# Optimization experiments

Hardware: AMD Instinct MI355X
Metric: run time of the kernel (lower is better)

The kernel has to match this reference:

```python
import jax, jax.numpy as jnp
import numpy as np

# Module hyperparameters (from init_kwargs)
NBITS = 8
FOLD = 8
B = 8192
IN_F = 2048
OUT_F = 2048
ISIZE = IN_F // FOLD   # 256
OSIZE = OUT_F // FOLD  # 256
QMAX = 2 ** (NBITS - 1) - 1  # 127


def setup_inputs() -> dict:
    key = jax.random.key(0)
    k1, k2, k3, k4, k5 = jax.random.split(key, 5)
    inp = jax.random.normal(k1, (B, IN_F), dtype=jnp.float32)
    # per-fold linear weights, torch nn.Linear default-ish scale
    W = jax.random.normal(k2, (FOLD, OSIZE, ISIZE), dtype=jnp.float32) * (1.0 / np.sqrt(ISIZE))
    # UniformPositionalEncoding buffers: offset + per-fold per-column ranges
    pe = jax.random.normal(k3, (1, FOLD, ISIZE), dtype=jnp.float32) * 0.1
    min_range = -jax.random.uniform(k4, (1, FOLD, ISIZE), minval=0.25, maxval=1.0, dtype=jnp.float32)
    max_range = jax.random.uniform(k5, (1, FOLD, ISIZE), minval=0.25, maxval=1.0, dtype=jnp.float32)
    return {"input": inp, "W": W, "pe": pe, "min_range": min_range, "max_range": max_range}


def reference(input, W, pe, min_range, max_range):
    b = input.shape[0]
    x = input.reshape(b, FOLD, ISIZE)
    # QuantAct symmetric, clamp_only=True: per-tensor scale s = max|x| / n, clamp to [-s*n, s*n]
    s = jnp.max(jnp.abs(x)) / QMAX
    x = jnp.clip(x, -s * QMAX, s * QMAX)
    s = s * QMAX  # scaled range multiplier
    # positional offset, broadcast over batch
    x = x + pe[0]  # [b, FOLD, ISIZE]
    x_flat = x.reshape(b * FOLD, ISIZE)

    def per_fold(Wi, mn, mx):
        # fold_idx_ste forward passes full x through; range mask zeroes out-of-range entries
        mask = (x_flat < mn * s) | (x_flat > mx * s)  # [b*FOLD, ISIZE]
        xm = jnp.where(mask, jnp.float32(0.0), x_flat)
        o = xm @ Wi.T  # [b*FOLD, OSIZE]
        return o.reshape(b, FOLD, OSIZE).sum(axis=1)  # [b, OSIZE]

    # vmap over the FOLD small linears
    out = jax.vmap(per_fold)(W, min_range[0], max_range[0])  # [FOLD, b, OSIZE]
    out = jnp.transpose(out, (1, 0, 2)).reshape(b, FOLD * OSIZE)  # stack dim=1 then flatten
    return out
```

## Files before the change

### kernel.cpp

```cpp
#include <hip/hip_runtime.h>

#define FOLD  8
#define ISIZE 256
#define IN_F  2048
#define OUT_F 2048
#define TBM   32
#define NBLK  (8192 / TBM)
#define CHW   1104

typedef __attribute__((ext_vector_type(8))) short short8;
typedef __attribute__((ext_vector_type(4))) float f32x4;
typedef __attribute__((ext_vector_type(2))) float f32x2;

__device__ __forceinline__ unsigned f2bf(float f) {
    unsigned u = __float_as_uint(f);
    u += 0x7FFFu + ((u >> 16) & 1u);
    return (u >> 16);
}

__global__ __launch_bounds__(256)
void absmax_conv(const float* __restrict__ in,
                 const float* __restrict__ W,
                 float* __restrict__ partials,
                 unsigned short* __restrict__ wsw,
                 int quota) {
    const int nthreads = gridDim.x * 256;
    const int idx = blockIdx.x * 256 + threadIdx.x;

    if (blockIdx.x < 256) {
        const int t    = blockIdx.x * 256 + threadIdx.x;
        const int wid  = t >> 6;
        const int l    = t & 63;
        const int i  = wid >> 7;
        const int nt = (wid >> 3) & 15;
        const int ks = wid & 7;
        const int n = l & 15, q = l >> 4;
        const float* src = W + (((size_t)i * 256 + nt * 16 + n) * 256 + ks * 32 + q * 8);
        float4 s0 = *(const float4*)(src);
        float4 s1 = *(const float4*)(src + 4);
        uint4 p;
        p.x = f2bf(s0.x) | (f2bf(s0.y) << 16);
        p.y = f2bf(s0.z) | (f2bf(s0.w) << 16);
        p.z = f2bf(s1.x) | (f2bf(s1.y) << 16);
        p.w = f2bf(s1.z) | (f2bf(s1.w) << 16);
        *(uint4*)(wsw + (size_t)wid * 512 + l * 8) = p;
    }

    float m = 0.f;
    #pragma unroll 4
    for (int q = 0; q < quota; ++q) {
        f32x4 a = __builtin_nontemporal_load(
            (const f32x4*)(in + (size_t)(idx + q * nthreads) * 4));
        m = fmaxf(m, fmaxf(fmaxf(fabsf(a[0]), fabsf(a[1])),
                           fmaxf(fabsf(a[2]), fabsf(a[3]))));
    }
    #pragma unroll
    for (int off = 32; off > 0; off >>= 1)
        m = fmaxf(m, __shfl_down(m, off, 64));
    __shared__ float sm[4];
    int lane = threadIdx.x & 63, wv = threadIdx.x >> 6;
    if (lane == 0) sm[wv] = m;
    __syncthreads();
    if (threadIdx.x == 0)
        partials[blockIdx.x] = fmaxf(fmaxf(sm[0], sm[1]), fmaxf(sm[2], sm[3]));
}

__global__ __launch_bounds__(256)
void absmax_kernel(const float4* __restrict__ in,
                   float* __restrict__ partials,
                   unsigned int* __restrict__ scal,
                   int quota, int mode) {
    const int nthreads = gridDim.x * 256;
    const int idx = blockIdx.x * 256 + threadIdx.x;
    float m = 0.f;
    #pragma unroll 4
    for (int q = 0; q < quota; ++q) {
        float4 a = in[idx + q * nthreads];
        m = fmaxf(m, fmaxf(fmaxf(fabsf(a.x), fabsf(a.y)),
                           fmaxf(fabsf(a.z), fabsf(a.w))));
    }
    #pragma unroll
    for (int off = 32; off > 0; off >>= 1)
        m = fmaxf(m, __shfl_down(m, off, 64));
    __shared__ float sm[4];
    int lane = threadIdx.x & 63, wv = threadIdx.x >> 6;
    if (lane == 0) sm[wv] = m;
    __syncthreads();
    if (threadIdx.x == 0) {
        float r = fmaxf(fmaxf(sm[0], sm[1]), fmaxf(sm[2], sm[3]));
        if (mode) partials[blockIdx.x] = r;
        else      atomicMax(scal, __float_as_uint(r));
    }
}

__global__ __launch_bounds__(1024, 1)
void fold_nt(const float* __restrict__ in,
             const unsigned short* __restrict__ wsw,
             const float* __restrict__ pe,
             const float* __restrict__ mn,
             const float* __restrict__ mx,
             const float* __restrict__ partials,
             int npart,
             float* __restrict__ out) {
    __shared__ __align__(16) unsigned short ylds[64 * CHW];
    __shared__ float sred[16];

    const int tid  = threadIdx.x;
    const int lane = tid & 63;
    const int wv   = tid >> 6;
    const int row0 = blockIdx.x * TBM;

    float mabs;
    {
        float v = (tid < npart) ? partials[tid] : 0.0f;
        #pragma unroll
        for (int off = 32; off > 0; off >>= 1)
            v = fmaxf(v, __shfl_down(v, off, 64));
        if (lane == 0) sred[wv] = v;
        __syncthreads();
        float r = sred[0];
        #pragma unroll
        for (int i = 1; i < 16; ++i) r = fmaxf(r, sred[i]);
        mabs = r;
    }
    const float c = (mabs / 127.0f) * 127.0f;

    {
        const int kp  = tid & 127;
        const int rq  = tid >> 7;
        const int k0  = kp * 2;
        const int jh  = kp & 3;
        const int qA  = (kp >> 2) & 3;
        const int ksA = kp >> 4;

        float pef[FOLD][2], lo[FOLD][2], hi[FOLD][2];
        #pragma unroll
        for (int f = 0; f < FOLD; ++f) {
            float2 p2 = *(const float2*)(pe + f * ISIZE + k0);
            pef[f][0] = p2.x; pef[f][1] = p2.y;
        }
        #pragma unroll
        for (int i = 0; i < FOLD; ++i) {
            float2 a2 = *(const float2*)(mn + i * ISIZE + k0);
            float2 b2 = *(const float2*)(mx + i * ISIZE + k0);
            lo[i][0] = a2.x * c; lo[i][1] = a2.y * c;
            hi[i][0] = b2.x * c; hi[i][1] = b2.y * c;
        }

        #pragma unroll
        for (int r4 = 0; r4 < 4; ++r4) {
            const int row = rq * 4 + r4;
            const float* rowp = in + (size_t)(row0 + row) * IN_F + k0;
            f32x2 xr[FOLD];
            #pragma unroll
            for (int f = 0; f < FOLD; ++f)
                xr[f] = __builtin_nontemporal_load((const f32x2*)(rowp + f * ISIZE));

            float acc[FOLD][2];
            #pragma unroll
            for (int i = 0; i < FOLD; ++i) { acc[i][0] = 0.0f; acc[i][1] = 0.0f; }
            #pragma unroll
            for (int f = 0; f < FOLD; ++f) {
                float xv0 = fminf(fmaxf(xr[f][0], -c), c) + pef[f][0];
                float xv1 = fminf(fmaxf(xr[f][1], -c), c) + pef[f][1];
                #pragma unroll
                for (int i = 0; i < FOLD; ++i) {
                    if (xv0 >= lo[i][0] && xv0 <= hi[i][0]) acc[i][0] += xv0;
                    if (xv1 >= lo[i][1] && xv1 <= hi[i][1]) acc[i][1] += xv1;
                }
            }
            const unsigned base = (unsigned)((row >> 4) * 544 + qA * 136 + (row & 15) * 8 + jh * 2);
            #pragma unroll
            for (int i = 0; i < FOLD; ++i) {
                unsigned us = f2bf(acc[i][0]) | (f2bf(acc[i][1]) << 16);
                *(unsigned*)&ylds[(i * 8 + ksA) * CHW + base] = us;
            }
        }
    }
    __syncthreads();

    {
        const int fi   = wv >> 1;
        const int nh   = wv & 1;
        const int mrow = lane & 15;
        const int quad = lane >> 4;

        short8 afr[8][2];
        #pragma unroll
        for (int kk = 0; kk < 8; ++kk) {
            #pragma unroll
            for (int mt = 0; mt < 2; ++mt)
                afr[kk][mt] = *(const short8*)&ylds[(fi * 8 + kk) * CHW + mt * 544 + quad * 136 + mrow * 8];
        }

        const int col0 = fi * 256 + mrow;
        #pragma unroll 2
        for (int nt8 = 0; nt8 < 8; ++nt8) {
            const int ntg = nh * 8 + nt8;
            f32x4 a0 = (f32x4){0.f, 0.f, 0.f, 0.f};
            f32x4 a1 = (f32x4){0.f, 0.f, 0.f, 0.f};
            const unsigned short* wb = wsw + ((size_t)(fi * 16 + ntg) * 8) * 512 + lane * 8;
            uint4 wq[8];
            #pragma unroll
            for (int kk = 0; kk < 8; ++kk) wq[kk] = *(const uint4*)(wb + kk * 512);
            #pragma unroll
            for (int kk = 0; kk < 8; ++kk) {
                union { uint4 u; short8 s; } cv; cv.u = wq[kk];
                a0 = __builtin_amdgcn_mfma_f32_16x16x32_bf16(afr[kk][0], cv.s, a0, 0, 0, 0);
                a1 = __builtin_amdgcn_mfma_f32_16x16x32_bf16(afr[kk][1], cv.s, a1, 0, 0, 0);
            }
            #pragma unroll
            for (int rg = 0; rg < 4; ++rg) {
                __builtin_nontemporal_store(a0[rg],
                    &out[(size_t)(row0 +      quad * 4 + rg) * OUT_F + col0 + ntg * 16]);
                __builtin_nontemporal_store(a1[rg],
                    &out[(size_t)(row0 + 16 + quad * 4 + rg) * OUT_F + col0 + ntg * 16]);
            }
        }
    }
}

__global__ __launch_bounds__(1024, 1)
void fold_main(const float* __restrict__ in,
               const float* __restrict__ W,
               const float* __restrict__ pe,
               const float* __restrict__ mn,
               const float* __restrict__ mx,
               const float* __restrict__ partials,
               const unsigned int* __restrict__ scal,
               int npart,
               float* __restrict__ out) {
    __shared__ __align__(16) unsigned short ylds[64 * CHW];
    __shared__ float sred[16];

    const int tid  = threadIdx.x;
    const int lane = tid & 63;
    const int wv   = tid >> 6;
    const int row0 = blockIdx.x * TBM;

    float mabs;
    if (npart > 0) {
        float v = (tid < npart) ? partials[tid] : 0.0f;
        #pragma unroll
        for (int off = 32; off > 0; off >>= 1)
            v = fmaxf(v, __shfl_down(v, off, 64));
        if (lane == 0) sred[wv] = v;
        __syncthreads();
        float r = sred[0];
        #pragma unroll
        for (int i = 1; i < 16; ++i) r = fmaxf(r, sred[i]);
        mabs = r;
    } else {
        mabs = __uint_as_float(*scal);
    }
    const float c = (mabs / 127.0f) * 127.0f;

    {
        const int kp  = tid & 127;
        const int rq  = tid >> 7;
        const int k0  = kp * 2;
        const int jh  = kp & 3;
        const int qA  = (kp >> 2) & 3;
        const int ksA = kp >> 4;

        float pef[FOLD][2], lo[FOLD][2], hi[FOLD][2];
        #pragma unroll
        for (int f = 0; f < FOLD; ++f) {
            float2 p2 = *(const float2*)(pe + f * ISIZE + k0);
            pef[f][0] = p2.x; pef[f][1] = p2.y;
        }
        #pragma unroll
        for (int i = 0; i < FOLD; ++i) {
            float2 a2 = *(const float2*)(mn + i * ISIZE + k0);
            float2 b2 = *(const float2*)(mx + i * ISIZE + k0);
            lo[i][0] = a2.x * c; lo[i][1] = a2.y * c;
            hi[i][0] = b2.x * c; hi[i][1] = b2.y * c;
        }

        #pragma unroll
        for (int r4 = 0; r4 < 4; ++r4) {
            const int row = rq * 4 + r4;
            const float* rowp = in + (size_t)(row0 + row) * IN_F + k0;
            float2 xr[FOLD];
            #pragma unroll
            for (int f = 0; f < FOLD; ++f) xr[f] = *(const float2*)(rowp + f * ISIZE);

            float acc[FOLD][2];
            #pragma unroll
            for (int i = 0; i < FOLD; ++i) { acc[i][0] = 0.0f; acc[i][1] = 0.0f; }
            #pragma unroll
            for (int f = 0; f < FOLD; ++f) {
                float xv0 = fminf(fmaxf(xr[f].x, -c), c) + pef[f][0];
                float xv1 = fminf(fmaxf(xr[f].y, -c), c) + pef[f][1];
                #pragma unroll
                for (int i = 0; i < FOLD; ++i) {
                    if (xv0 >= lo[i][0] && xv0 <= hi[i][0]) acc[i][0] += xv0;
                    if (xv1 >= lo[i][1] && xv1 <= hi[i][1]) acc[i][1] += xv1;
                }
            }
            const unsigned base = (unsigned)((row >> 4) * 544 + qA * 136 + (row & 15) * 8 + jh * 2);
            #pragma unroll
            for (int i = 0; i < FOLD; ++i) {
                unsigned us = f2bf(acc[i][0]) | (f2bf(acc[i][1]) << 16);
                *(unsigned*)&ylds[(i * 8 + ksA) * CHW + base] = us;
            }
        }
    }
    __syncthreads();

    {
        const int fi   = wv >> 1;
        const int nh   = wv & 1;
        const int mrow = lane & 15;
        const int quad = lane >> 4;

        short8 afr[8][2];
        #pragma unroll
        for (int kk = 0; kk < 8; ++kk) {
            #pragma unroll
            for (int mt = 0; mt < 2; ++mt)
                afr[kk][mt] = *(const short8*)&ylds[(fi * 8 + kk) * CHW + mt * 544 + quad * 136 + mrow * 8];
        }

        const int col0 = fi * 256 + mrow;
        #pragma unroll 2
        for (int nt8 = 0; nt8 < 8; ++nt8) {
            const int ntg = nh * 8 + nt8;
            f32x4 a0 = (f32x4){0.f, 0.f, 0.f, 0.f};
            f32x4 a1 = (f32x4){0.f, 0.f, 0.f, 0.f};
            const float* wb = W + ((size_t)(fi * 256 + ntg * 16 + mrow) * 256 + quad * 8);
            float4 w[16];
            #pragma unroll
            for (int kk = 0; kk < 8; ++kk) {
                w[2 * kk]     = *(const float4*)(wb + kk * 32);
                w[2 * kk + 1] = *(const float4*)(wb + kk * 32 + 4);
            }
            #pragma unroll
            for (int kk = 0; kk < 8; ++kk) {
                union { uint4 u; short8 s; } cv;
                cv.u.x = f2bf(w[2*kk].x)   | (f2bf(w[2*kk].y)   << 16);
                cv.u.y = f2bf(w[2*kk].z)   | (f2bf(w[2*kk].w)   << 16);
                cv.u.z = f2bf(w[2*kk+1].x) | (f2bf(w[2*kk+1].y) << 16);
                cv.u.w = f2bf(w[2*kk+1].z) | (f2bf(w[2*kk+1].w) << 16);
                a0 = __builtin_amdgcn_mfma_f32_16x16x32_bf16(afr[kk][0], cv.s, a0, 0, 0, 0);
                a1 = __builtin_amdgcn_mfma_f32_16x16x32_bf16(afr[kk][1], cv.s, a1, 0, 0, 0);
            }
            #pragma unroll
            for (int rg = 0; rg < 4; ++rg) {
                out[(size_t)(row0 +      quad * 4 + rg) * OUT_F + col0 + ntg * 16] = a0[rg];
                out[(size_t)(row0 + 16 + quad * 4 + rg) * OUT_F + col0 + ntg * 16] = a1[rg];
            }
        }
    }
}

extern "C" void kernel_launch(void* const* d_in, const int* in_sizes, int n_in,
                              void* d_out, int out_size, void* d_ws, size_t ws_size,
                              hipStream_t stream) {
    const float* in = (const float*)d_in[0];
    const float* W  = (const float*)d_in[1];
    const float* pe = (const float*)d_in[2];
    const float* mn = (const float*)d_in[3];
    const float* mx = (const float*)d_in[4];
    float* out = (float*)d_out;

    const size_t PART_OFF  = 16;
    const size_t WSW_OFF   = 8192;
    const size_t WSW_BYTES = (size_t)FOLD * 256 * 256 * 2;

    unsigned int*   scal     = (unsigned int*)d_ws;
    float*          partials = (float*)((char*)d_ws + PART_OFF);
    unsigned short* wsw      = (unsigned short*)((char*)d_ws + WSW_OFF);

    const bool preconv = ws_size >= WSW_OFF + WSW_BYTES;

    if (preconv && ws_size >= PART_OFF + 1024 * sizeof(float)) {
        absmax_conv<<<1024, 256, 0, stream>>>(in, W, partials, wsw, 16);
        fold_nt<<<NBLK, 1024, 0, stream>>>(in, wsw, pe, mn, mx, partials, 1024, out);
        return;
    }

    int npart;
    if (ws_size >= PART_OFF + 1024 * sizeof(float)) {
        absmax_kernel<<<1024, 256, 0, stream>>>((const float4*)in, partials, scal, 16, 1);
        npart = 1024;
    } else if (ws_size >= PART_OFF + 256 * sizeof(float)) {
        absmax_kernel<<<256, 256, 0, stream>>>((const float4*)in, partials, scal, 64, 1);
        npart = 256;
    } else {
        (void)hipMemsetAsync(d_ws, 0, sizeof(unsigned int), stream);
        absmax_kernel<<<256, 256, 0, stream>>>((const float4*)in, partials, scal, 64, 0);
        npart = 0;
    }
    fold_main<<<NBLK, 1024, 0, stream>>>(in, W, pe, mn, mx,
                                         partials, scal, npart, out);
}
```

Measured before the change: 155.1 us.

## Split fold kernel into two 16-row halves with prefetch overlapping MFMA phase

The fused fold kernel now processes its 32-row tile as two 16-row halves in separate LDS buffers. Input rows for the second half are prefetched into registers before the first half's MFMA/store phase, then masked and converted after it. The aim is to overlap global input loads with matrix work and output stores instead of running them back to back. In exchange each weight tile is loaded twice per block, there is an extra barrier, and range parameters are reloaded, which raises register pressure.

```diff
diff --git a/kernel.cpp b/kernel.cpp
--- a/kernel.cpp
+++ b/kernel.cpp
@@ -7,6 +7,8 @@
 #define TBM   32
 #define NBLK  (8192 / TBM)
 #define CHW   1104
+#define CHW2  560
+#define HALFY (64 * CHW2)
 
 typedef __attribute__((ext_vector_type(8))) short short8;
 typedef __attribute__((ext_vector_type(4))) float f32x4;
@@ -93,16 +95,93 @@
     }
 }
 
+__device__ __forceinline__ void load_params(const float* __restrict__ pe,
+                                            const float* __restrict__ mn,
+                                            const float* __restrict__ mx,
+                                            int k0, float c,
+                                            float (*pef)[2], float (*lo)[2],
+                                            float (*hi)[2]) {
+    #pragma unroll
+    for (int f = 0; f < FOLD; ++f) {
+        float2 p2 = *(const float2*)(pe + f * ISIZE + k0);
+        pef[f][0] = p2.x; pef[f][1] = p2.y;
+    }
+    #pragma unroll
+    for (int i = 0; i < FOLD; ++i) {
+        float2 a2 = *(const float2*)(mn + i * ISIZE + k0);
+        float2 b2 = *(const float2*)(mx + i * ISIZE + k0);
+        lo[i][0] = a2.x * c; lo[i][1] = a2.y * c;
+        hi[i][0] = b2.x * c; hi[i][1] = b2.y * c;
+    }
+}
+
+__device__ __forceinline__ void a_row(const f32x2* __restrict__ xr,
+                                      const float (*pef)[2], const float (*lo)[2],
+                                      const float (*hi)[2], float c,
+                                      unsigned short* __restrict__ yh,
+                                      int row16, int jh, int qA, int ksA) {
+    float acc[FOLD][2];
+    #pragma unroll
+    for (int i = 0; i < FOLD; ++i) { acc[i][0] = 0.0f; acc[i][1] = 0.0f; }
+    #pragma unroll
+    for (int f = 0; f < FOLD; ++f) {
+        float xv0 = fminf(fmaxf(xr[f][0], -c), c) + pef[f][0];
+        float xv1 = fminf(fmaxf(xr[f][1], -c), c) + pef[f][1];
+        #pragma unroll
+        for (int i = 0; i < FOLD; ++i) {
+            if (xv0 >= lo[i][0] && xv0 <= hi[i][0]) acc[i][0] += xv0;
+            if (xv1 >= lo[i][1] && xv1 <= hi[i][1]) acc[i][1] += xv1;
+        }
+    }
+    const unsigned base = (unsigned)(qA * 136 + row16 * 8 + jh * 2);
+    #pragma unroll
+    for (int i = 0; i < FOLD; ++i) {
+        unsigned us = f2bf(acc[i][0]) | (f2bf(acc[i][1]) << 16);
+        *(unsigned*)&yh[(i * 8 + ksA) * CHW2 + base] = us;
+    }
+}
+
+__device__ __forceinline__ void b_half(const unsigned short* __restrict__ yh,
+                                       const unsigned short* __restrict__ wsw,
+                                       float* __restrict__ out,
+                                       int row0h, int fi, int nh,
+                                       int mrow, int quad, int lane) {
+    short8 afr[8];
+    #pragma unroll
+    for (int kk = 0; kk < 8; ++kk)
+        afr[kk] = *(const short8*)&yh[(fi * 8 + kk) * CHW2 + quad * 136 + mrow * 8];
+
+    const int col0 = fi * 256 + mrow;
+    #pragma unroll 2
+    for (int nt8 = 0; nt8 < 8; ++nt8) {
+        const int ntg = nh * 8 + nt8;
+        f32x4 a0 = (f32x4){0.f, 0.f, 0.f, 0.f};
+        const unsigned short* wb = wsw + ((size_t)(fi * 16 + ntg) * 8) * 512 + lane * 8;
+        uint4 wq[8];
+        #pragma unroll
+        for (int kk = 0; kk < 8; ++kk) wq[kk] = *(const uint4*)(wb + kk * 512);
+        #pragma unroll
+        for (int kk = 0; kk < 8; ++kk) {
+            union { uint4 u; short8 s; } cv; cv.u = wq[kk];
+            a0 = __builtin_amdgcn_mfma_f32_16x16x32_bf16(afr[kk], cv.s, a0, 0, 0, 0);
+        }
+        #pragma unroll
+        for (int rg = 0; rg < 4; ++rg)
+            __builtin_nontemporal_store(a0[rg],
+                &out[(size_t)(row0h + quad * 4 + rg) * OUT_F + col0 + ntg * 16]);
+    }
+}
+
 __global__ __launch_bounds__(1024, 1)
-void fold_nt(const float* __restrict__ in,
-             const unsigned short* __restrict__ wsw,
-             const float* __restrict__ pe,
-             const float* __restrict__ mn,
-             const float* __restrict__ mx,
-             const float* __restrict__ partials,
-             int npart,
-             float* __restrict__ out) {
-    __shared__ __align__(16) unsigned short ylds[64 * CHW];
+void fold_pipe(const float* __restrict__ in,
+               const unsigned short* __restrict__ wsw,
+               const float* __restrict__ pe,
+               const float* __restrict__ mn,
+               const float* __restrict__ mx,
+               const float* __restrict__ partials,
+               int npart,
+               float* __restrict__ out) {
+    __shared__ __align__(16) unsigned short ylds[2][HALFY];
     __shared__ float sred[16];
 
     const int tid  = threadIdx.x;
@@ -125,99 +204,56 @@
     }
     const float c = (mabs / 127.0f) * 127.0f;
 
+    const int kp  = tid & 127;
+    const int rq  = tid >> 7;
+    const int k0  = kp * 2;
+    const int jh  = kp & 3;
+    const int qA  = (kp >> 2) & 3;
+    const int ksA = kp >> 4;
+
+    const int fi   = wv >> 1;
+    const int nh   = wv & 1;
+    const int mrow = lane & 15;
+    const int quad = lane >> 4;
+
     {
-        const int kp  = tid & 127;
-        const int rq  = tid >> 7;
-        const int k0  = kp * 2;
-        const int jh  = kp & 3;
-        const int qA  = (kp >> 2) & 3;
-        const int ksA = kp >> 4;
-
         float pef[FOLD][2], lo[FOLD][2], hi[FOLD][2];
-        #pragma unroll
-        for (int f = 0; f < FOLD; ++f) {
-            float2 p2 = *(const float2*)(pe + f * ISIZE + k0);
-            pef[f][0] = p2.x; pef[f][1] = p2.y;
-        }
-        #pragma unroll
-        for (int i = 0; i < FOLD; ++i) {
-            float2 a2 = *(const float2*)(mn + i * ISIZE + k0);
-            float2 b2 = *(const float2*)(mx + i * ISIZE + k0);
-            lo[i][0] = a2.x * c; lo[i][1] = a2.y * c;
-            hi[i][0] = b2.x * c; hi[i][1] = b2.y * c;
-        }
-
-        #pragma unroll
-        for (int r4 = 0; r4 < 4; ++r4) {
-            const int row = rq * 4 + r4;
-            const float* rowp = in + (size_t)(row0 + row) * IN_F + k0;
+        load_params(pe, mn, mx, k0, c, pef, lo, hi);
+        #pragma unroll
+        for (int r2 = 0; r2 < 2; ++r2) {
+            const int row16 = rq * 2 + r2;
+            const float* rowp = in + (size_t)(row0 + row16) * IN_F + k0;
             f32x2 xr[FOLD];
             #pragma unroll
             for (int f = 0; f < FOLD; ++f)
                 xr[f] = __builtin_nontemporal_load((const f32x2*)(rowp + f * ISIZE));
-
-            float acc[FOLD][2];
-            #pragma unroll
-            for (int i = 0; i < FOLD; ++i) { acc[i][0] = 0.0f; acc[i][1] = 0.0f; }
-            #pragma unroll
-            for (int f = 0; f < FOLD; ++f) {
-                float xv0 = fminf(fmaxf(xr[f][0], -c), c) + pef[f][0];
-                float xv1 = fminf(fmaxf(xr[f][1], -c), c) + pef[f][1];
-                #pragma unroll
-                for (int i = 0; i < FOLD; ++i) {
-                    if (xv0 >= lo[i][0] && xv0 <= hi[i][0]) acc[i][0] += xv0;
-                    if (xv1 >= lo[i][1] && xv1 <= hi[i][1]) acc[i][1] += xv1;
-                }
-            }
-            const unsigned base = (unsigned)((row >> 4) * 544 + qA * 136 + (row & 15) * 8 + jh * 2);
-            #pragma unroll
-            for (int i = 0; i < FOLD; ++i) {
-                unsigned us = f2bf(acc[i][0]) | (f2bf(acc[i][1]) << 16);
-                *(unsigned*)&ylds[(i * 8 + ksA) * CHW + base] = us;
-            }
+            a_row(xr, pef, lo, hi, c, ylds[0], row16, jh, qA, ksA);
         }
     }
     __syncthreads();
 
+    f32x2 xpre[2][FOLD];
+    #pragma unroll
+    for (int r2 = 0; r2 < 2; ++r2) {
+        const int row16 = rq * 2 + r2;
+        const float* rowp = in + (size_t)(row0 + 16 + row16) * IN_F + k0;
+        #pragma unroll
+        for (int f = 0; f < FOLD; ++f)
+            xpre[r2][f] = __builtin_nontemporal_load((const f32x2*)(rowp + f * ISIZE));
+    }
+
+    b_half(ylds[0], wsw, out, row0, fi, nh, mrow, quad, lane);
+
     {
-        const int fi   = wv >> 1;
-        const int nh   = wv & 1;
-        const int mrow = lane & 15;
-        const int quad = lane >> 4;
-
-        short8 afr[8][2];
-        #pragma unroll
-        for (int kk = 0; kk < 8; ++kk) {
-            #pragma unroll
-            for (int mt = 0; mt < 2; ++mt)
-                afr[kk][mt] = *(const short8*)&ylds[(fi * 8 + kk) * CHW + mt * 544 + quad * 136 + mrow * 8];
-        }
-
-        const int col0 = fi * 256 + mrow;
-        #pragma unroll 2
-        for (int nt8 = 0; nt8 < 8; ++nt8) {
-            const int ntg = nh * 8 + nt8;
-            f32x4 a0 = (f32x4){0.f, 0.f, 0.f, 0.f};
-            f32x4 a1 = (f32x4){0.f, 0.f, 0.f, 0.f};
-            const unsigned short* wb = wsw + ((size_t)(fi * 16 + ntg) * 8) * 512 + lane * 8;
-            uint4 wq[8];
-            #pragma unroll
-            for (int kk = 0; kk < 8; ++kk) wq[kk] = *(const uint4*)(wb + kk * 512);
-            #pragma unroll
-            for (int kk = 0; kk < 8; ++kk) {
-                union { uint4 u; short8 s; } cv; cv.u = wq[kk];
-                a0 = __builtin_amdgcn_mfma_f32_16x16x32_bf16(afr[kk][0], cv.s, a0, 0, 0, 0);
-                a1 = __builtin_amdgcn_mfma_f32_16x16x32_bf16(afr[kk][1], cv.s, a1, 0, 0, 0);
-            }
-            #pragma unroll
-            for (int rg = 0; rg < 4; ++rg) {
-                __builtin_nontemporal_store(a0[rg],
-                    &out[(size_t)(row0 +      quad * 4 + rg) * OUT_F + col0 + ntg * 16]);
-                __builtin_nontemporal_store(a1[rg],
-                    &out[(size_t)(row0 + 16 + quad * 4 + rg) * OUT_F + col0 + ntg * 16]);
-            }
-        }
-    }
+        float pef[FOLD][2], lo[FOLD][2], hi[FOLD][2];
+        load_params(pe, mn, mx, k0, c, pef, lo, hi);
+        #pragma unroll
+        for (int r2 = 0; r2 < 2; ++r2)
+            a_row(xpre[r2], pef, lo, hi, c, ylds[1], rq * 2 + r2, jh, qA, ksA);
+    }
+    __syncthreads();
+
+    b_half(ylds[1], wsw, out, row0 + 16, fi, nh, mrow, quad, lane);
 }
 
 __global__ __launch_bounds__(1024, 1)
@@ -376,7 +412,7 @@
 
     if (preconv && ws_size >= PART_OFF + 1024 * sizeof(float)) {
         absmax_conv<<<1024, 256, 0, stream>>>(in, W, partials, wsw, 16);
-        fold_nt<<<NBLK, 1024, 0, stream>>>(in, wsw, pe, mn, mx, partials, 1024, out);
+        fold_pipe<<<NBLK, 1024, 0, stream>>>(in, wsw, pe, mn, mx, partials, 1024, out);
         return;
     }
 
```

Result: slower. 181.0 us (+16.7%).
